# Optimization experiments

Measured on AMD Instinct MI355X. Metric: run time of the kernel, lower is better.

The kernel has to match this reference:

```python
import jax, jax.numpy as jnp
import numpy as np

T = 32  # timesteps


def _conv(x, w, pad):
    # x: NCHW, w: OIHW
    return jax.lax.conv_general_dilated(
        x, w, window_strides=(1, 1), padding=[(pad, pad), (pad, pad)],
        dimension_numbers=("NCHW", "OIHW", "NCHW"))


def setup_inputs() -> dict:
    key = jax.random.key(0)
    ks = jax.random.split(key, 10)
    K, D, Cin = 64, 512, 1024
    x = jax.random.normal(ks[0], (256, Cin, 14, 14), dtype=jnp.float32)
    # xavier-ish scales
    redu_w = jax.random.normal(ks[1], (D, Cin, 1, 1), jnp.float32) * (2.0 / (D + Cin)) ** 0.5
    redu_b = jax.random.uniform(ks[2], (D,), jnp.float32)
    share_w = jax.random.normal(ks[3], (K, D, 1, 1), jnp.float32) * (2.0 / (K + D)) ** 0.5
    share_b = jax.random.uniform(ks[4], (K,), jnp.float32)
    fan = K * 9
    U_z = jax.random.normal(ks[5], (K, K, 3, 3), jnp.float32) * (2.0 / (fan + fan)) ** 0.5
    U_r = jax.random.normal(ks[6], (K, K, 3, 3), jnp.float32) * (2.0 / (fan + fan)) ** 0.5
    U_h = jax.random.normal(ks[7], (K, K, 3, 3), jnp.float32) * (2.0 / (fan + fan)) ** 0.5
    lim = (6.0 / (K + D)) ** 0.5
    centers = jax.random.uniform(ks[8], (K, D), jnp.float32, -lim, lim)
    return {"x": x, "redu_w": redu_w, "redu_b": redu_b, "share_w": share_w,
            "share_b": share_b, "U_z": U_z, "U_r": U_r, "U_h": U_h,
            "centers": centers}


def reference(x, redu_w, redu_b, share_w, share_b, U_z, U_r, U_h, centers):
    NT, _, H, W = x.shape
    B = NT // T
    K, D = centers.shape
    # 1x1 channel reduction (with_relu=False)
    xr = _conv(x, redu_w, 0) + redu_b[None, :, None, None]          # (B*T, D, H, W)
    wxb = _conv(xr, share_w, 0) + share_b[None, :, None, None]      # (B*T, K, H, W)
    wxb = wxb.reshape(B, T, K, H, W).transpose(1, 0, 2, 3, 4)       # (T, B, K, H, W)

    def step(h, wt):
        z = jax.nn.sigmoid(wt + _conv(h, U_z, 1))
        r = jax.nn.sigmoid(wt + _conv(h, U_r, 1))
        hh = jnp.tanh(wt + _conv(r * h, U_h, 1))
        h = (1.0 - z) * hh + z * h
        return h, h

    h0 = jnp.zeros((B, K, H, W), x.dtype)
    _, fwd = jax.lax.scan(step, h0, wxb)                 # (T, B, K, H, W)
    _, bwd = jax.lax.scan(step, h0, wxb, reverse=True)   # already re-reversed order
    assign = (fwd + bwd).transpose(1, 0, 2, 3, 4).reshape(B * T, K, H * W)
    assign = jax.nn.softmax(assign, axis=1)              # softmax over centers per pixel

    a = assign.sum(-1, keepdims=True) * centers[None]    # (B*T, K, D)
    xt = xr.reshape(B * T, D, H * W)
    vlad = jnp.einsum("bkp,bdp->bkd", assign, xt) - a    # (B*T, K, D)
    vlad = vlad.reshape(B, T, K, D).sum(axis=1)          # (B, K, D)
    vlad = vlad / jnp.clip(jnp.linalg.norm(vlad, axis=2, keepdims=True), 1e-12)
    vlad = vlad.reshape(B, K * D)
    vlad = vlad / jnp.clip(jnp.linalg.norm(vlad, axis=1, keepdims=True), 1e-12)
    return vlad
```

## Files before the change

kernel.cpp:

```cpp
#include <hip/hip_runtime.h>

#define HW 196
#define WIDTH 14
#define T_STEPS 32
#define KC 64
#define DD 512
#define CIN 1024
#define NFR 256
#define NB 8
#define NCOL (NFR * HW)

using f16x8 = __attribute__((ext_vector_type(8))) _Float16;
using f16x4 = __attribute__((ext_vector_type(4))) _Float16;
using f32x4 = __attribute__((ext_vector_type(4))) float;

__device__ __forceinline__ void gload_lds16(const void* g, void* l) {
  __builtin_amdgcn_global_load_lds(
      (const __attribute__((address_space(1))) void*)g,
      (__attribute__((address_space(3))) void*)l, 16, 0, 0);
}

__device__ __forceinline__ float sigf(float x) {
  return __builtin_amdgcn_rcpf(1.0f + __expf(-x));
}
__device__ __forceinline__ float tanhfast(float x) {
  float e = __expf(2.0f * x);
  return 1.0f - 2.0f * __builtin_amdgcn_rcpf(e + 1.0f);
}

__global__ __launch_bounds__(256)
void cvt_f16(const float* __restrict__ src, _Float16* __restrict__ dst, int nelem) {
  int i = (blockIdx.x * 256 + threadIdx.x) * 4;
  if (i < nelem) {
    float4 v = *reinterpret_cast<const float4*>(src + i);
    f16x4 o;
    o[0] = (_Float16)v.x; o[1] = (_Float16)v.y;
    o[2] = (_Float16)v.z; o[3] = (_Float16)v.w;
    *reinterpret_cast<f16x4*>(dst + i) = o;
  }
}

__global__ __launch_bounds__(256)
void transpose_x(const float* __restrict__ x, _Float16* __restrict__ xh) {
  __shared__ float tile[64][197];
  const int tid = threadIdx.x;
  const int w = tid >> 6, lane = tid & 63;
  const int n = blockIdx.y;
  const int c0 = blockIdx.x * 64;
  const float* src = x + ((size_t)n * CIN + c0) * HW;
  for (int rr = 0; rr < 16; ++rr) {
    int c = w * 16 + rr;
    if (lane < 49) {
      float4 v = *reinterpret_cast<const float4*>(src + (size_t)c * HW + lane * 4);
      tile[c][lane * 4 + 0] = v.x; tile[c][lane * 4 + 1] = v.y;
      tile[c][lane * 4 + 2] = v.z; tile[c][lane * 4 + 3] = v.w;
    }
  }
  __syncthreads();
  _Float16* dst = xh + (size_t)n * HW * CIN + c0;
  #pragma unroll
  for (int pass = 0; pass < 13; ++pass) {
    int p = (tid >> 4) + pass * 16;
    int cg = (tid & 15) * 4;
    if (p < HW) {
      f16x4 v;
      #pragma unroll
      for (int j = 0; j < 4; ++j) v[j] = (_Float16)tile[cg + j][p];
      *reinterpret_cast<f16x4*>(dst + (size_t)p * CIN + cg) = v;
    }
  }
}

template<int BM, int NMT, bool WT>
__global__ __launch_bounds__(256)
void gemm16(const _Float16* __restrict__ A, const _Float16* __restrict__ Bmat,
            const float* __restrict__ bias, float* __restrict__ outC,
            _Float16* __restrict__ outT, int M, int K) {
  constexpr int MF = BM / 32;
  union Smem {
    struct { _Float16 a[BM * 64]; _Float16 b[128 * 64]; } s;
    _Float16 t[WT ? 128 * 132 : 1];
  };
  __shared__ Smem u;

  const int tid = threadIdx.x;
  const int lane = tid & 63;
  const int w = tid >> 6;
  const int wm = w >> 1, wn = w & 1;
  const int l16 = lane & 15, lhi = lane >> 4;
  const int srow = lane >> 3, sslot = lane & 7;
  const int swz = (sslot ^ srow) << 4;
  const int nct = gridDim.x / NMT;
  const int mt = blockIdx.x / nct;
  const int ct = blockIdx.x - mt * nct;
  const int m0 = mt * BM;
  const int col0 = ct * 128;

  f32x4 acc[MF][4];
  #pragma unroll
  for (int i = 0; i < MF; ++i)
    #pragma unroll
    for (int f = 0; f < 4; ++f) acc[i][f] = {0.f, 0.f, 0.f, 0.f};

  for (int k0 = 0; k0 < K; k0 += 64) {
    #pragma unroll
    for (int s = 0; s < BM / 32; ++s) {
      int r = w * (BM / 4) + s * 8;
      gload_lds16((const char*)(A + (size_t)(m0 + r + srow) * K + k0) + swz,
                  (char*)u.s.a + r * 128);
    }
    #pragma unroll
    for (int s = 0; s < 4; ++s) {
      int r = w * 32 + s * 8;
      gload_lds16((const char*)(Bmat + (size_t)(col0 + r + srow) * K + k0) + swz,
                  (char*)u.s.b + r * 128);
    }
    __syncthreads();
    #pragma unroll
    for (int kk = 0; kk < 2; ++kk) {
      f16x8 af[MF];
      #pragma unroll
      for (int i = 0; i < MF; ++i) {
        int row = wm * (MF * 16) + i * 16 + l16;
        af[i] = *reinterpret_cast<const f16x8*>(
            (const char*)u.s.a + row * 128 + ((kk * 64 + lhi * 16) ^ ((row & 7) << 4)));
      }
      #pragma unroll
      for (int f = 0; f < 4; ++f) {
        int row = wn * 64 + f * 16 + l16;
        f16x8 bf = *reinterpret_cast<const f16x8*>(
            (const char*)u.s.b + row * 128 + ((kk * 64 + lhi * 16) ^ ((row & 7) << 4)));
        #pragma unroll
        for (int i = 0; i < MF; ++i)
          acc[i][f] = __builtin_amdgcn_mfma_f32_16x16x32_f16(af[i], bf, acc[i][f], 0, 0, 0);
      }
    }
    __syncthreads();
  }

  if constexpr (!WT) {
    #pragma unroll
    for (int i = 0; i < MF; ++i) {
      int m = m0 + wm * (MF * 16) + i * 16 + lhi * 4;
      float b0 = bias[m], b1 = bias[m + 1], b2 = bias[m + 2], b3 = bias[m + 3];
      #pragma unroll
      for (int f = 0; f < 4; ++f) {
        int col = col0 + wn * 64 + f * 16 + l16;
        float4 o = {acc[i][f][0] + b0, acc[i][f][1] + b1,
                    acc[i][f][2] + b2, acc[i][f][3] + b3};
        *reinterpret_cast<float4*>(outC + (size_t)col * M + m) = o;
      }
    }
  } else {
    #pragma unroll
    for (int i = 0; i < MF; ++i) {
      int ml = wm * (MF * 16) + i * 16 + lhi * 4;
      int m = m0 + ml;
      float b0 = bias[m], b1 = bias[m + 1], b2 = bias[m + 2], b3 = bias[m + 3];
      #pragma unroll
      for (int f = 0; f < 4; ++f) {
        int cl = wn * 64 + f * 16 + l16;
        f16x4 v;
        v[0] = (_Float16)(acc[i][f][0] + b0);
        v[1] = (_Float16)(acc[i][f][1] + b1);
        v[2] = (_Float16)(acc[i][f][2] + b2);
        v[3] = (_Float16)(acc[i][f][3] + b3);
        *reinterpret_cast<f16x4*>((char*)u.t + cl * 264 + ml * 2) = v;
      }
    }
    __syncthreads();
    #pragma unroll
    for (int pass = 0; pass < 16; ++pass) {
      int row = (tid >> 5) + pass * 8;
      int coff = (tid & 31) * 4;
      f16x4 v = *reinterpret_cast<const f16x4*>((const char*)u.t + row * 264 + coff * 2);
      *reinterpret_cast<f16x4*>(outT + (size_t)(col0 + row) * M + m0 + coff) = v;
    }
  }
}

__global__ __launch_bounds__(64)
void format_u(const float* __restrict__ Uz, const float* __restrict__ Ur,
              const float* __restrict__ Uh, _Float16* __restrict__ ufmt) {
  const int f = blockIdx.x;
  const int lane = threadIdx.x;
  const int l16 = lane & 15;
  const float* U;
  int ch, kt;
  if (f < 144) {
    int pair = f / 36, rem = f - pair * 36;
    int mi = rem / 18; kt = rem - mi * 18;
    U = (pair < 2) ? Uz : Ur;
    ch = (pair & 1) * 32 + mi * 16 + l16;
  } else {
    int g = f - 144;
    int pair = g / 36, rem = g - pair * 36;
    int mi = rem / 18; kt = rem - mi * 18;
    U = Uh;
    ch = pair * 32 + mi * 16 + l16;
  }
  const int tap = kt >> 1;
  const int k0 = (kt & 1) * 32 + (lane >> 4) * 8;
  f16x8 v;
  #pragma unroll
  for (int j = 0; j < 8; ++j)
    v[j] = (_Float16)U[(size_t)ch * 576 + (k0 + j) * 9 + tap];
  *reinterpret_cast<f16x8*>(ufmt + (size_t)f * 512 + lane * 8) = v;
}

__global__ __launch_bounds__(512, 2)
void gru_mfma8(const float* __restrict__ wxbc, const _Float16* __restrict__ ufmt,
               _Float16* __restrict__ a_f, _Float16* __restrict__ a_b) {
  __shared__ __align__(16) _Float16 hpad[256 * 64];
  __shared__ __align__(16) _Float16 rhpad[256 * 64];
  __shared__ __align__(16) _Float16 zbuf[208 * 64];
  __shared__ __align__(16) float h32[HW * 68];

  const int tid = threadIdx.x;
  const int lane = tid & 63;
  const int w = tid >> 6;
  const int l16 = lane & 15, lhi = lane >> 4;
  const int chain = blockIdx.x;
  const int b = chain >> 1, dir = chain & 1;
  const int mi = w & 3;
  const int half = w >> 2;
  const int ntb = half * 7;
  const int ntn = half ? 6 : 7;
  const int ch0 = mi * 16 + lhi * 4;
  const int chlo = lhi * 16, chhi = 64 + lhi * 16;

  for (int i = tid; i < 256 * 64; i += 512) { hpad[i] = (_Float16)0.f; rhpad[i] = (_Float16)0.f; }
  for (int i = tid; i < HW * 68; i += 512) h32[i] = 0.0f;
  __syncthreads();

  _Float16* adest = dir ? a_b : a_f;
  const char* hpadB = reinterpret_cast<const char*>(hpad);
  const char* rhpadB = reinterpret_cast<const char*>(rhpad);
  const _Float16* uf = ufmt + (size_t)lane * 8;
  const int fz0 = (mi >> 1) * 36 + (mi & 1) * 18;

  for (int t = 0; t < T_STEPS; ++t) {
    const int tw = dir ? (T_STEPS - 1 - t) : t;
    const float* wtc = wxbc + (size_t)(b * T_STEPS + tw) * HW * KC;

    {
      f16x8 afz[18], afr[18];
      #pragma unroll
      for (int kt = 0; kt < 18; ++kt) {
        afz[kt] = *reinterpret_cast<const f16x8*>(uf + (size_t)(fz0 + kt) * 512);
        afr[kt] = *reinterpret_cast<const f16x8*>(uf + (size_t)(fz0 + 72 + kt) * 512);
      }
      for (int i = 0; i < ntn; ++i) {
        const int nt = ntb + i;
        const int p = nt * 16 + l16;
        const bool act = p < HW;
        const int pc = act ? p : (HW - 1);
        const int py = pc / 14, px_ = pc - py * 14;
        const int base0 = py * 16 + px_;
        const int tb = base0 * 128;
        const int rb0 = tb +       (chlo ^ ((px_ & 7) << 4));
        const int rb1 = tb + 128 + (chlo ^ (((px_ + 1) & 7) << 4));
        const int rb2 = tb + 256 + (chlo ^ (((px_ + 2) & 7) << 4));
        const int rb3 = tb +       (chhi ^ ((px_ & 7) << 4));
        const int rb4 = tb + 128 + (chhi ^ (((px_ + 1) & 7) << 4));
        const int rb5 = tb + 256 + (chhi ^ (((px_ + 2) & 7) << 4));
        const float4 wt4 = *reinterpret_cast<const float4*>(wtc + (size_t)pc * KC + ch0);
        f32x4 az = {0.f, 0.f, 0.f, 0.f};
        f32x4 ar = {0.f, 0.f, 0.f, 0.f};
        #pragma unroll
        for (int kt = 0; kt < 18; ++kt) {
          const int tap = kt >> 1, dy = tap / 3, dx = tap - dy * 3;
          const int base = (kt & 1) ? (dx == 0 ? rb3 : dx == 1 ? rb4 : rb5)
                                    : (dx == 0 ? rb0 : dx == 1 ? rb1 : rb2);
          const f16x8 bf = *reinterpret_cast<const f16x8*>(hpadB + base + dy * 2048);
          az = __builtin_amdgcn_mfma_f32_16x16x32_f16(afz[kt], bf, az, 0, 0, 0);
          ar = __builtin_amdgcn_mfma_f32_16x16x32_f16(afr[kt], bf, ar, 0, 0, 0);
        }
        if (act) {
          const float wta[4] = {wt4.x, wt4.y, wt4.z, wt4.w};
          const float4 hv = *reinterpret_cast<const float4*>(&h32[pc * 68 + ch0]);
          const float hva[4] = {hv.x, hv.y, hv.z, hv.w};
          f16x4 zw, rhw;
          #pragma unroll
          for (int jj = 0; jj < 4; ++jj) {
            float z = sigf(az[jj] + wta[jj]);
            float r = sigf(ar[jj] + wta[jj]);
            zw[jj] = (_Float16)z;
            rhw[jj] = (_Float16)(r * hva[jj]);
          }
          *reinterpret_cast<f16x4*>(reinterpret_cast<char*>(zbuf) +
              p * 128 + ((ch0 * 2) ^ ((p & 7) << 4))) = zw;
          const int ppw = base0 + 17;
          *reinterpret_cast<f16x4*>(reinterpret_cast<char*>(rhpad) +
              ppw * 128 + ((ch0 * 2) ^ ((ppw & 7) << 4))) = rhw;
        }
      }
    }
    __syncthreads();

    {
      _Float16* ad = adest + (size_t)(b * T_STEPS + tw) * HW * KC;
      f16x8 afh[18];
      #pragma unroll
      for (int kt = 0; kt < 18; ++kt)
        afh[kt] = *reinterpret_cast<const f16x8*>(uf + (size_t)(144 + fz0 + kt) * 512);
      for (int i = 0; i < ntn; ++i) {
        const int nt = ntb + i;
        const int p = nt * 16 + l16;
        const bool act = p < HW;
        const int pc = act ? p : (HW - 1);
        const int py = pc / 14, px_ = pc - py * 14;
        const int base0 = py * 16 + px_;
        const int tb = base0 * 128;
        const int rb0 = tb +       (chlo ^ ((px_ & 7) << 4));
        const int rb1 = tb + 128 + (chlo ^ (((px_ + 1) & 7) << 4));
        const int rb2 = tb + 256 + (chlo ^ (((px_ + 2) & 7) << 4));
        const int rb3 = tb +       (chhi ^ ((px_ & 7) << 4));
        const int rb4 = tb + 128 + (chhi ^ (((px_ + 1) & 7) << 4));
        const int rb5 = tb + 256 + (chhi ^ (((px_ + 2) & 7) << 4));
        const float4 wt4 = *reinterpret_cast<const float4*>(wtc + (size_t)pc * KC + ch0);
        f32x4 ah = {0.f, 0.f, 0.f, 0.f};
        #pragma unroll
        for (int kt = 0; kt < 18; ++kt) {
          const int tap = kt >> 1, dy = tap / 3, dx = tap - dy * 3;
          const int base = (kt & 1) ? (dx == 0 ? rb3 : dx == 1 ? rb4 : rb5)
                                    : (dx == 0 ? rb0 : dx == 1 ? rb1 : rb2);
          const f16x8 bf = *reinterpret_cast<const f16x8*>(rhpadB + base + dy * 2048);
          ah = __builtin_amdgcn_mfma_f32_16x16x32_f16(afh[kt], bf, ah, 0, 0, 0);
        }
        if (act) {
          const float wta[4] = {wt4.x, wt4.y, wt4.z, wt4.w};
          const f16x4 zv = *reinterpret_cast<const f16x4*>(
              reinterpret_cast<const char*>(zbuf) + p * 128 + ((ch0 * 2) ^ ((p & 7) << 4)));
          const float4 hv = *reinterpret_cast<const float4*>(&h32[pc * 68 + ch0]);
          const float hva[4] = {hv.x, hv.y, hv.z, hv.w};
          f16x4 hw;
          float hna[4];
          #pragma unroll
          for (int jj = 0; jj < 4; ++jj) {
            float hh = tanhfast(ah[jj] + wta[jj]);
            float z = (float)zv[jj];
            float hn = hh + z * (hva[jj] - hh);
            hna[jj] = hn;
            hw[jj] = (_Float16)hn;
          }
          float4 hn4 = {hna[0], hna[1], hna[2], hna[3]};
          *reinterpret_cast<float4*>(&h32[pc * 68 + ch0]) = hn4;
          const int ppw = base0 + 17;
          *reinterpret_cast<f16x4*>(reinterpret_cast<char*>(hpad) +
              ppw * 128 + ((ch0 * 2) ^ ((ppw & 7) << 4))) = hw;
          *reinterpret_cast<f16x4*>(ad + (size_t)pc * KC + ch0) = hw;
        }
      }
    }
    __syncthreads();
  }
}

__global__ __launch_bounds__(256)
void softmax_kernel(const _Float16* __restrict__ af, const _Float16* __restrict__ ab,
                    _Float16* __restrict__ out) {
  size_t idx = (size_t)blockIdx.x * 256 + threadIdx.x;
  const _Float16* cf = af + idx * KC;
  const _Float16* cb = ab + idx * KC;
  _Float16* co = out + idx * KC;
  float v[KC];
  float mx = -3.4e38f;
  #pragma unroll
  for (int g = 0; g < 8; ++g) {
    f16x8 a = *reinterpret_cast<const f16x8*>(cf + g * 8);
    f16x8 bq = *reinterpret_cast<const f16x8*>(cb + g * 8);
    #pragma unroll
    for (int j = 0; j < 8; ++j) {
      float s = (float)a[j] + (float)bq[j];
      v[g * 8 + j] = s;
      mx = fmaxf(mx, s);
    }
  }
  float ssum = 0.0f;
  #pragma unroll
  for (int k = 0; k < KC; ++k) { v[k] = __expf(v[k] - mx); ssum += v[k]; }
  float inv = __builtin_amdgcn_rcpf(ssum);
  #pragma unroll
  for (int g = 0; g < 8; ++g) {
    f16x8 o;
    #pragma unroll
    for (int j = 0; j < 8; ++j) o[j] = (_Float16)(v[g * 8 + j] * inv);
    *reinterpret_cast<f16x8*>(co + g * 8) = o;
  }
}

__global__ __launch_bounds__(256)
void sreduce_kernel(const _Float16* __restrict__ a, float* __restrict__ S) {
  __shared__ float red[4][64];
  const int seg = blockIdx.x, b = blockIdx.y, tid = threadIdx.x;
  const int k = tid & 63, rg = tid >> 6;
  const _Float16* base = a + (size_t)b * T_STEPS * HW * KC;
  float sum = 0.0f;
  for (int rr = seg * 784 + rg; rr < (seg + 1) * 784; rr += 4)
    sum += (float)base[(size_t)rr * KC + k];
  red[rg][k] = sum;
  __syncthreads();
  if (tid < 64) {
    float s = red[0][k] + red[1][k] + red[2][k] + red[3][k];
    atomicAdd(&S[b * KC + k], s);
  }
}

__global__ __launch_bounds__(256)
void vlad_gemm_kernel(const _Float16* __restrict__ a, const _Float16* __restrict__ xrh,
                      float* __restrict__ Gpart) {
  __shared__ float sA[16][68];
  __shared__ float sX[16][68];
  const int tid = threadIdx.x;
  const int tx = tid & 15, ty = tid >> 4;
  const int d0 = blockIdx.x * 64;
  const int tc = blockIdx.y;
  const int b  = blockIdx.z;
  const int kk = tid & 63, pj = tid >> 6;
  float acc[4][4] = {};

  for (int tt = 0; tt < 4; ++tt) {
    int n = b * T_STEPS + tc * 4 + tt;
    const _Float16* an = a + (size_t)n * HW * KC;
    const _Float16* xn = xrh + (size_t)n * HW * DD;
    for (int p0 = 0; p0 < HW; p0 += 16) {
      __syncthreads();
      #pragma unroll
      for (int j = 0; j < 4; ++j) {
        int pl = pj * 4 + j;
        int p = p0 + pl;
        sA[pl][kk] = (p < HW) ? (float)an[(size_t)p * KC + kk] : 0.0f;
        sX[pl][kk] = (p < HW) ? (float)xn[(size_t)p * DD + d0 + kk] : 0.0f;
      }
      __syncthreads();
      #pragma unroll
      for (int pp = 0; pp < 16; ++pp) {
        float4 av = *reinterpret_cast<const float4*>(&sA[pp][ty * 4]);
        float4 xv = *reinterpret_cast<const float4*>(&sX[pp][tx * 4]);
        float aa[4] = {av.x, av.y, av.z, av.w};
        float xx[4] = {xv.x, xv.y, xv.z, xv.w};
        #pragma unroll
        for (int i = 0; i < 4; ++i)
          #pragma unroll
          for (int j = 0; j < 4; ++j)
            acc[i][j] += aa[i] * xx[j];
      }
    }
  }
  float* gp = Gpart + ((size_t)(tc * NB + b) * KC) * DD;
  #pragma unroll
  for (int i = 0; i < 4; ++i)
    #pragma unroll
    for (int j = 0; j < 4; ++j)
      gp[(ty * 4 + i) * DD + d0 + tx * 4 + j] = acc[i][j];
}

__global__ __launch_bounds__(256)
void finalize1_kernel(const float* __restrict__ Gpart, const float* __restrict__ S,
                      const float* __restrict__ centers, float* __restrict__ out,
                      float* __restrict__ bsum) {
  __shared__ float red[256];
  const int k = blockIdx.x, b = blockIdx.y, tid = threadIdx.x;
  const float sv = S[b * KC + k];
  float vals[2];
  float ss = 0.0f;
  #pragma unroll
  for (int r = 0; r < 2; ++r) {
    int d = tid + r * 256;
    float g = 0.0f;
    #pragma unroll
    for (int tc = 0; tc < 8; ++tc)
      g += Gpart[((size_t)(tc * NB + b) * KC + k) * DD + d];
    float v = g - sv * centers[k * DD + d];
    vals[r] = v; ss += v * v;
  }
  red[tid] = ss; __syncthreads();
  for (int st = 128; st > 0; st >>= 1) {
    if (tid < st) red[tid] += red[tid + st];
    __syncthreads();
  }
  float tot = red[0];
  float inv = 1.0f / fmaxf(sqrtf(tot), 1e-12f);
  #pragma unroll
  for (int r = 0; r < 2; ++r) {
    int d = tid + r * 256;
    out[(size_t)b * KC * DD + k * DD + d] = vals[r] * inv;
  }
  if (tid == 0) atomicAdd(&bsum[b], tot * inv * inv);
}

__global__ __launch_bounds__(256)
void finalize2_kernel(float* __restrict__ out, const float* __restrict__ bsum) {
  int idx = blockIdx.x * 256 + threadIdx.x;
  int b = idx >> 15;
  out[idx] = out[idx] / fmaxf(sqrtf(bsum[b]), 1e-12f);
}

extern "C" void kernel_launch(void* const* d_in, const int* in_sizes, int n_in,
                              void* d_out, int out_size, void* d_ws, size_t ws_size,
                              hipStream_t stream) {
  const float* x       = (const float*)d_in[0];
  const float* redu_w  = (const float*)d_in[1];
  const float* redu_b  = (const float*)d_in[2];
  const float* share_w = (const float*)d_in[3];
  const float* share_b = (const float*)d_in[4];
  const float* Uz      = (const float*)d_in[5];
  const float* Ur      = (const float*)d_in[6];
  const float* Uh      = (const float*)d_in[7];
  const float* centers = (const float*)d_in[8];
  float* out = (float*)d_out;

  float* wxbc = (float*)d_ws;
  _Float16* assignh = (_Float16*)wxbc;
  _Float16* xh = (_Float16*)(wxbc + (size_t)NCOL * KC);
  _Float16* a_f = xh;
  _Float16* a_b = a_f + (size_t)NFR * HW * KC;
  float* Gpart = (float*)(a_b + (size_t)NFR * HW * KC);
  _Float16* xrh = xh + (size_t)NCOL * CIN;
  float* S = (float*)(xrh + (size_t)NCOL * DD);
  float* bsum = S + 512;
  _Float16* ufmt = (_Float16*)(bsum + 8);
  _Float16* wh = ufmt + 216 * 512;
  _Float16* swh = wh + (size_t)DD * CIN;

  hipMemsetAsync(bsum, 0, NB * sizeof(float), stream);
  hipMemsetAsync(S, 0, 512 * sizeof(float), stream);

  cvt_f16<<<dim3(512), 256, 0, stream>>>(redu_w, wh, DD * CIN);
  cvt_f16<<<dim3(32), 256, 0, stream>>>(share_w, swh, KC * DD);
  format_u<<<dim3(216), 64, 0, stream>>>(Uz, Ur, Uh, ufmt);
  transpose_x<<<dim3(16, 256), 256, 0, stream>>>(x, xh);

  gemm16<128, 4, true><<<dim3(392 * 4), 256, 0, stream>>>(
      wh, xh, redu_b, nullptr, xrh, DD, CIN);
  gemm16<64, 1, false><<<dim3(392), 256, 0, stream>>>(
      swh, xrh, share_b, wxbc, nullptr, KC, DD);

  gru_mfma8<<<dim3(16), 512, 0, stream>>>(wxbc, ufmt, a_f, a_b);

  softmax_kernel<<<dim3(196), 256, 0, stream>>>(a_f, a_b, assignh);
  sreduce_kernel<<<dim3(8, 8), 256, 0, stream>>>(assignh, S);
  vlad_gemm_kernel<<<dim3(8, 8, 8), 256, 0, stream>>>(assignh, xrh, Gpart);
  finalize1_kernel<<<dim3(64, 8), 256, 0, stream>>>(Gpart, S, centers, out, bsum);
  finalize2_kernel<<<dim3(1024), 256, 0, stream>>>(out, bsum);
}
```

Baseline: 773.7 us.

## Switch GRU recurrence to 32x32x16 MFMA tiles with streamed weight fragments

Rewrites the per-timestep GRU convolutions to use 32x32x16 MFMA instructions over 32-pixel tiles instead of 16x16x32 over 16-pixel tiles. The U weights are repacked to match the new fragment layout. Weight fragments are now loaded from global memory inside the K loop instead of being held in registers. The goal is more work per MFMA and fewer LDS reads of the hidden state on the serial critical path, at the cost of repeated weight loads that must hit cache and a different split of waves across tiles (8 waves over 7 tiles with some idle).

```diff
diff --git a/kernel.cpp b/kernel.cpp
--- a/kernel.cpp
+++ b/kernel.cpp
@@ -13,6 +13,7 @@
 using f16x8 = __attribute__((ext_vector_type(8))) _Float16;
 using f16x4 = __attribute__((ext_vector_type(4))) _Float16;
 using f32x4 = __attribute__((ext_vector_type(4))) float;
+using f32x16 = __attribute__((ext_vector_type(16))) float;
 
 __device__ __forceinline__ void gload_lds16(const void* g, void* l) {
   __builtin_amdgcn_global_load_lds(
@@ -180,27 +181,18 @@
 }
 
 __global__ __launch_bounds__(64)
-void format_u(const float* __restrict__ Uz, const float* __restrict__ Ur,
-              const float* __restrict__ Uh, _Float16* __restrict__ ufmt) {
+void format_u32(const float* __restrict__ Uz, const float* __restrict__ Ur,
+                const float* __restrict__ Uh, _Float16* __restrict__ ufmt) {
   const int f = blockIdx.x;
   const int lane = threadIdx.x;
-  const int l16 = lane & 15;
-  const float* U;
-  int ch, kt;
-  if (f < 144) {
-    int pair = f / 36, rem = f - pair * 36;
-    int mi = rem / 18; kt = rem - mi * 18;
-    U = (pair < 2) ? Uz : Ur;
-    ch = (pair & 1) * 32 + mi * 16 + l16;
-  } else {
-    int g = f - 144;
-    int pair = g / 36, rem = g - pair * 36;
-    int mi = rem / 18; kt = rem - mi * 18;
-    U = Uh;
-    ch = pair * 32 + mi * 16 + l16;
-  }
-  const int tap = kt >> 1;
-  const int k0 = (kt & 1) * 32 + (lane >> 4) * 8;
+  const int g = f / 72;
+  const int rem = f - g * 72;
+  const int mig = rem / 36;
+  const int kt = rem - mig * 36;
+  const int tap = kt >> 2, chq = kt & 3;
+  const float* U = (g == 0) ? Uz : (g == 1) ? Ur : Uh;
+  const int ch = mig * 32 + (lane & 31);
+  const int k0 = chq * 16 + (lane >> 5) * 8;
   f16x8 v;
   #pragma unroll
   for (int j = 0; j < 8; ++j)
@@ -209,25 +201,22 @@
 }
 
 __global__ __launch_bounds__(512, 2)
-void gru_mfma8(const float* __restrict__ wxbc, const _Float16* __restrict__ ufmt,
-               _Float16* __restrict__ a_f, _Float16* __restrict__ a_b) {
+void gru32(const float* __restrict__ wxbc, const _Float16* __restrict__ ufmt,
+           _Float16* __restrict__ a_f, _Float16* __restrict__ a_b) {
   __shared__ __align__(16) _Float16 hpad[256 * 64];
   __shared__ __align__(16) _Float16 rhpad[256 * 64];
-  __shared__ __align__(16) _Float16 zbuf[208 * 64];
+  __shared__ __align__(16) _Float16 zbuf[HW * 64];
   __shared__ __align__(16) float h32[HW * 68];
 
   const int tid = threadIdx.x;
   const int lane = tid & 63;
   const int w = tid >> 6;
-  const int l16 = lane & 15, lhi = lane >> 4;
+  const int l31 = lane & 31, lhalf = lane >> 5;
   const int chain = blockIdx.x;
   const int b = chain >> 1, dir = chain & 1;
-  const int mi = w & 3;
-  const int half = w >> 2;
-  const int ntb = half * 7;
-  const int ntn = half ? 6 : 7;
-  const int ch0 = mi * 16 + lhi * 4;
-  const int chlo = lhi * 16, chhi = 64 + lhi * 16;
+  const int mig = w & 1;
+  const int q = w >> 1;
+  const int kl16 = lhalf * 16;
 
   for (int i = tid; i < 256 * 64; i += 512) { hpad[i] = (_Float16)0.f; rhpad[i] = (_Float16)0.f; }
   for (int i = tid; i < HW * 68; i += 512) h32[i] = 0.0f;
@@ -237,119 +226,125 @@
   const char* hpadB = reinterpret_cast<const char*>(hpad);
   const char* rhpadB = reinterpret_cast<const char*>(rhpad);
   const _Float16* uf = ufmt + (size_t)lane * 8;
-  const int fz0 = (mi >> 1) * 36 + (mi & 1) * 18;
+  const int fzz = mig * 36;
+  const int fzr = 72 + mig * 36;
+  const int fzh = 144 + mig * 36;
 
   for (int t = 0; t < T_STEPS; ++t) {
     const int tw = dir ? (T_STEPS - 1 - t) : t;
     const float* wtc = wxbc + (size_t)(b * T_STEPS + tw) * HW * KC;
 
+    for (int it = 0; it < 2; ++it) {
+      const int nt = q + 4 * it;
+      if (nt >= 7) break;
+      const int p = nt * 32 + l31;
+      const bool act = p < HW;
+      const int pc = act ? p : (HW - 1);
+      const int py = pc / 14, px_ = pc - py * 14;
+      const int base0 = py * 16 + px_;
+      const int tb = base0 * 128;
+      int rbq[12];
+      #pragma unroll
+      for (int dx = 0; dx < 3; ++dx) {
+        const int sw = ((base0 + dx) & 7) << 4;
+        #pragma unroll
+        for (int chq = 0; chq < 4; ++chq)
+          rbq[dx * 4 + chq] = tb + dx * 128 + ((chq * 32 + kl16) ^ sw);
+      }
+      f32x16 accz = {}, accr = {};
+      #pragma unroll
+      for (int kt = 0; kt < 36; ++kt) {
+        const int tap = kt >> 2, chq = kt & 3;
+        const int dy = tap / 3, dx = tap - dy * 3;
+        const f16x8 bf = *reinterpret_cast<const f16x8*>(
+            hpadB + rbq[dx * 4 + chq] + dy * 2048);
+        const f16x8 az = *reinterpret_cast<const f16x8*>(uf + (size_t)(fzz + kt) * 512);
+        const f16x8 ar = *reinterpret_cast<const f16x8*>(uf + (size_t)(fzr + kt) * 512);
+        accz = __builtin_amdgcn_mfma_f32_32x32x16_f16(az, bf, accz, 0, 0, 0);
+        accr = __builtin_amdgcn_mfma_f32_32x32x16_f16(ar, bf, accr, 0, 0, 0);
+      }
+      if (act) {
+        const int ppw = base0 + 17;
+        #pragma unroll
+        for (int rq = 0; rq < 4; ++rq) {
+          const int ch = mig * 32 + rq * 8 + lhalf * 4;
+          const float4 wt4 = *reinterpret_cast<const float4*>(wtc + (size_t)pc * KC + ch);
+          const float4 hv = *reinterpret_cast<const float4*>(&h32[pc * 68 + ch]);
+          const float wta[4] = {wt4.x, wt4.y, wt4.z, wt4.w};
+          const float hva[4] = {hv.x, hv.y, hv.z, hv.w};
+          f16x4 zw, rhw;
+          #pragma unroll
+          for (int jj = 0; jj < 4; ++jj) {
+            float z = sigf(accz[rq * 4 + jj] + wta[jj]);
+            float r = sigf(accr[rq * 4 + jj] + wta[jj]);
+            zw[jj] = (_Float16)z;
+            rhw[jj] = (_Float16)(r * hva[jj]);
+          }
+          *reinterpret_cast<f16x4*>(reinterpret_cast<char*>(zbuf) +
+              p * 128 + ((ch * 2) ^ ((p & 7) << 4))) = zw;
+          *reinterpret_cast<f16x4*>(reinterpret_cast<char*>(rhpad) +
+              ppw * 128 + ((ch * 2) ^ ((ppw & 7) << 4))) = rhw;
+        }
+      }
+    }
+    __syncthreads();
+
     {
-      f16x8 afz[18], afr[18];
-      #pragma unroll
-      for (int kt = 0; kt < 18; ++kt) {
-        afz[kt] = *reinterpret_cast<const f16x8*>(uf + (size_t)(fz0 + kt) * 512);
-        afr[kt] = *reinterpret_cast<const f16x8*>(uf + (size_t)(fz0 + 72 + kt) * 512);
-      }
-      for (int i = 0; i < ntn; ++i) {
-        const int nt = ntb + i;
-        const int p = nt * 16 + l16;
+      _Float16* ad = adest + (size_t)(b * T_STEPS + tw) * HW * KC;
+      for (int it = 0; it < 2; ++it) {
+        const int nt = q + 4 * it;
+        if (nt >= 7) break;
+        const int p = nt * 32 + l31;
         const bool act = p < HW;
         const int pc = act ? p : (HW - 1);
         const int py = pc / 14, px_ = pc - py * 14;
         const int base0 = py * 16 + px_;
         const int tb = base0 * 128;
-        const int rb0 = tb +       (chlo ^ ((px_ & 7) << 4));
-        const int rb1 = tb + 128 + (chlo ^ (((px_ + 1) & 7) << 4));
-        const int rb2 = tb + 256 + (chlo ^ (((px_ + 2) & 7) << 4));
-        const int rb3 = tb +       (chhi ^ ((px_ & 7) << 4));
-        const int rb4 = tb + 128 + (chhi ^ (((px_ + 1) & 7) << 4));
-        const int rb5 = tb + 256 + (chhi ^ (((px_ + 2) & 7) << 4));
-        const float4 wt4 = *reinterpret_cast<const float4*>(wtc + (size_t)pc * KC + ch0);
-        f32x4 az = {0.f, 0.f, 0.f, 0.f};
-        f32x4 ar = {0.f, 0.f, 0.f, 0.f};
+        int rbq[12];
         #pragma unroll
-        for (int kt = 0; kt < 18; ++kt) {
-          const int tap = kt >> 1, dy = tap / 3, dx = tap - dy * 3;
-          const int base = (kt & 1) ? (dx == 0 ? rb3 : dx == 1 ? rb4 : rb5)
-                                    : (dx == 0 ? rb0 : dx == 1 ? rb1 : rb2);
-          const f16x8 bf = *reinterpret_cast<const f16x8*>(hpadB + base + dy * 2048);
-          az = __builtin_amdgcn_mfma_f32_16x16x32_f16(afz[kt], bf, az, 0, 0, 0);
-          ar = __builtin_amdgcn_mfma_f32_16x16x32_f16(afr[kt], bf, ar, 0, 0, 0);
+        for (int dx = 0; dx < 3; ++dx) {
+          const int sw = ((base0 + dx) & 7) << 4;
+          #pragma unroll
+          for (int chq = 0; chq < 4; ++chq)
+            rbq[dx * 4 + chq] = tb + dx * 128 + ((chq * 32 + kl16) ^ sw);
+        }
+        f32x16 acch = {};
+        #pragma unroll
+        for (int kt = 0; kt < 36; ++kt) {
+          const int tap = kt >> 2, chq = kt & 3;
+          const int dy = tap / 3, dx = tap - dy * 3;
+          const f16x8 bf = *reinterpret_cast<const f16x8*>(
+              rhpadB + rbq[dx * 4 + chq] + dy * 2048);
+          const f16x8 ah = *reinterpret_cast<const f16x8*>(uf + (size_t)(fzh + kt) * 512);
+          acch = __builtin_amdgcn_mfma_f32_32x32x16_f16(ah, bf, acch, 0, 0, 0);
         }
         if (act) {
-          const float wta[4] = {wt4.x, wt4.y, wt4.z, wt4.w};
-          const float4 hv = *reinterpret_cast<const float4*>(&h32[pc * 68 + ch0]);
-          const float hva[4] = {hv.x, hv.y, hv.z, hv.w};
-          f16x4 zw, rhw;
+          const int ppw = base0 + 17;
           #pragma unroll
-          for (int jj = 0; jj < 4; ++jj) {
-            float z = sigf(az[jj] + wta[jj]);
-            float r = sigf(ar[jj] + wta[jj]);
-            zw[jj] = (_Float16)z;
-            rhw[jj] = (_Float16)(r * hva[jj]);
+          for (int rq = 0; rq < 4; ++rq) {
+            const int ch = mig * 32 + rq * 8 + lhalf * 4;
+            const float4 wt4 = *reinterpret_cast<const float4*>(wtc + (size_t)pc * KC + ch);
+            const f16x4 zv = *reinterpret_cast<const f16x4*>(
+                reinterpret_cast<const char*>(zbuf) + p * 128 + ((ch * 2) ^ ((p & 7) << 4)));
+            const float4 hv = *reinterpret_cast<const float4*>(&h32[pc * 68 + ch]);
+            const float wta[4] = {wt4.x, wt4.y, wt4.z, wt4.w};
+            const float hva[4] = {hv.x, hv.y, hv.z, hv.w};
+            f16x4 hw;
+            float hna[4];
+            #pragma unroll
+            for (int jj = 0; jj < 4; ++jj) {
+              float hh = tanhfast(acch[rq * 4 + jj] + wta[jj]);
+              float z = (float)zv[jj];
+              float hn = hh + z * (hva[jj] - hh);
+              hna[jj] = hn;
+              hw[jj] = (_Float16)hn;
+            }
+            float4 hn4 = {hna[0], hna[1], hna[2], hna[3]};
+            *reinterpret_cast<float4*>(&h32[pc * 68 + ch]) = hn4;
+            *reinterpret_cast<f16x4*>(reinterpret_cast<char*>(hpad) +
+                ppw * 128 + ((ch * 2) ^ ((ppw & 7) << 4))) = hw;
+            *reinterpret_cast<f16x4*>(ad + (size_t)pc * KC + ch) = hw;
           }
-          *reinterpret_cast<f16x4*>(reinterpret_cast<char*>(zbuf) +
-              p * 128 + ((ch0 * 2) ^ ((p & 7) << 4))) = zw;
-          const int ppw = base0 + 17;
-          *reinterpret_cast<f16x4*>(reinterpret_cast<char*>(rhpad) +
-              ppw * 128 + ((ch0 * 2) ^ ((ppw & 7) << 4))) = rhw;
-        }
-      }
-    }
-    __syncthreads();
-
-    {
-      _Float16* ad = adest + (size_t)(b * T_STEPS + tw) * HW * KC;
-      f16x8 afh[18];
-      #pragma unroll
-      for (int kt = 0; kt < 18; ++kt)
-        afh[kt] = *reinterpret_cast<const f16x8*>(uf + (size_t)(144 + fz0 + kt) * 512);
-      for (int i = 0; i < ntn; ++i) {
-        const int nt = ntb + i;
-        const int p = nt * 16 + l16;
-        const bool act = p < HW;
-        const int pc = act ? p : (HW - 1);
-        const int py = pc / 14, px_ = pc - py * 14;
-        const int base0 = py * 16 + px_;
-        const int tb = base0 * 128;
-        const int rb0 = tb +       (chlo ^ ((px_ & 7) << 4));
-        const int rb1 = tb + 128 + (chlo ^ (((px_ + 1) & 7) << 4));
-        const int rb2 = tb + 256 + (chlo ^ (((px_ + 2) & 7) << 4));
-        const int rb3 = tb +       (chhi ^ ((px_ & 7) << 4));
-        const int rb4 = tb + 128 + (chhi ^ (((px_ + 1) & 7) << 4));
-        const int rb5 = tb + 256 + (chhi ^ (((px_ + 2) & 7) << 4));
-        const float4 wt4 = *reinterpret_cast<const float4*>(wtc + (size_t)pc * KC + ch0);
-        f32x4 ah = {0.f, 0.f, 0.f, 0.f};
-        #pragma unroll
-        for (int kt = 0; kt < 18; ++kt) {
-          const int tap = kt >> 1, dy = tap / 3, dx = tap - dy * 3;
-          const int base = (kt & 1) ? (dx == 0 ? rb3 : dx == 1 ? rb4 : rb5)
-                                    : (dx == 0 ? rb0 : dx == 1 ? rb1 : rb2);
-          const f16x8 bf = *reinterpret_cast<const f16x8*>(rhpadB + base + dy * 2048);
-          ah = __builtin_amdgcn_mfma_f32_16x16x32_f16(afh[kt], bf, ah, 0, 0, 0);
-        }
-        if (act) {
-          const float wta[4] = {wt4.x, wt4.y, wt4.z, wt4.w};
-          const f16x4 zv = *reinterpret_cast<const f16x4*>(
-              reinterpret_cast<const char*>(zbuf) + p * 128 + ((ch0 * 2) ^ ((p & 7) << 4)));
-          const float4 hv = *reinterpret_cast<const float4*>(&h32[pc * 68 + ch0]);
-          const float hva[4] = {hv.x, hv.y, hv.z, hv.w};
-          f16x4 hw;
-          float hna[4];
-          #pragma unroll
-          for (int jj = 0; jj < 4; ++jj) {
-            float hh = tanhfast(ah[jj] + wta[jj]);
-            float z = (float)zv[jj];
-            float hn = hh + z * (hva[jj] - hh);
-            hna[jj] = hn;
-            hw[jj] = (_Float16)hn;
-          }
-          float4 hn4 = {hna[0], hna[1], hna[2], hna[3]};
-          *reinterpret_cast<float4*>(&h32[pc * 68 + ch0]) = hn4;
-          const int ppw = base0 + 17;
-          *reinterpret_cast<f16x4*>(reinterpret_cast<char*>(hpad) +
-              ppw * 128 + ((ch0 * 2) ^ ((ppw & 7) << 4))) = hw;
-          *reinterpret_cast<f16x4*>(ad + (size_t)pc * KC + ch0) = hw;
         }
       }
     }
@@ -529,7 +524,7 @@
 
   cvt_f16<<<dim3(512), 256, 0, stream>>>(redu_w, wh, DD * CIN);
   cvt_f16<<<dim3(32), 256, 0, stream>>>(share_w, swh, KC * DD);
-  format_u<<<dim3(216), 64, 0, stream>>>(Uz, Ur, Uh, ufmt);
+  format_u32<<<dim3(216), 64, 0, stream>>>(Uz, Ur, Uh, ufmt);
   transpose_x<<<dim3(16, 256), 256, 0, stream>>>(x, xh);
 
   gemm16<128, 4, true><<<dim3(392 * 4), 256, 0, stream>>>(
@@ -537,7 +532,7 @@
   gemm16<64, 1, false><<<dim3(392), 256, 0, stream>>>(
       swh, xrh, share_b, wxbc, nullptr, KC, DD);
 
-  gru_mfma8<<<dim3(16), 512, 0, stream>>>(wxbc, ufmt, a_f, a_b);
+  gru32<<<dim3(16), 512, 0, stream>>>(wxbc, ufmt, a_f, a_b);
 
   softmax_kernel<<<dim3(196), 256, 0, stream>>>(a_f, a_b, assignh);
   sreduce_kernel<<<dim3(8, 8), 256, 0, stream>>>(assignh, S);
```

Result: slower. 1.502 ms (+94.1%).
